# Kernel tuning notes

Hardware: AMD Instinct MI355X
Metric: run time of the kernel (lower is better)

## Reference

```python
import jax, jax.numpy as jnp
import numpy as np

N, F, H, E = 10000, 256, 256, 320000
TEMPERATURE = 1.0


def setup_inputs() -> dict:
    key = jax.random.key(0)
    k_x, k_ei, k_w1, k_b1, k_w2, k_b2 = jax.random.split(key, 6)
    x = jax.random.normal(k_x, (N, F), dtype=jnp.float32)
    edge_index = jax.random.randint(k_ei, (2, E), 0, N, dtype=jnp.int64)
    # PyTorch nn.Linear default init: U(-1/sqrt(fan_in), 1/sqrt(fan_in)), weight shape (out, in)
    lim1 = 1.0 / np.sqrt(2 * F)
    W1 = jax.random.uniform(k_w1, (H, 2 * F), dtype=jnp.float32, minval=-lim1, maxval=lim1)
    b1 = jax.random.uniform(k_b1, (H,), dtype=jnp.float32, minval=-lim1, maxval=lim1)
    lim2 = 1.0 / np.sqrt(H)
    W2 = jax.random.uniform(k_w2, (1, H), dtype=jnp.float32, minval=-lim2, maxval=lim2)
    b2 = jax.random.uniform(k_b2, (1,), dtype=jnp.float32, minval=-lim2, maxval=lim2)
    return {"x": x, "edge_index": edge_index, "W1": W1, "b1": b1, "W2": W2, "b2": b2}


def reference(x, edge_index, W1, b1, W2, b2):
    row, col = edge_index[0], edge_index[1]
    edge_feat = jnp.concatenate([x[row], x[col]], axis=-1)  # (E, 2F)
    h = jax.nn.relu(edge_feat @ W1.T + b1)                  # (E, H)
    logits = (h @ W2.T + b2).squeeze(-1)                    # (E,)
    m = jax.nn.sigmoid(logits / max(TEMPERATURE, 1e-6))
    return m
```

## Files before the change

### kernel.cpp

```cpp
#include <hip/hip_runtime.h>
#include <hip/hip_bf16.h>


typedef __attribute__((ext_vector_type(8))) short bf16x8;
typedef __attribute__((ext_vector_type(4))) float f32x4;
typedef __attribute__((ext_vector_type(2))) float f32x2;

__device__ __forceinline__ unsigned short f2bf(float f) {
    __hip_bfloat16 h = __float2bfloat16(f);
    return *reinterpret_cast<unsigned short*>(&h);
}

__device__ __forceinline__ unsigned char f2fp8(float f) {
    return (unsigned char)(__builtin_amdgcn_cvt_pk_fp8_f32(f, f, 0, false) & 0xff);
}

__global__ __launch_bounds__(256) void convert_w(const float* __restrict__ w1,
                                                 unsigned short* __restrict__ wb,
                                                 int nw4) {
    int i = blockIdx.x * 256 + threadIdx.x;
    if (i < nw4) {
        float4 v = ((const float4*)w1)[i];
        ushort4 o = {f2bf(v.x), f2bf(v.y), f2bf(v.z), f2bf(v.w)};
        ((ushort4*)wb)[i] = o;
    }
}

__global__ __launch_bounds__(256) void gemm_mfma(const float* __restrict__ x,
                                                 const unsigned short* __restrict__ wb,
                                                 const float* __restrict__ b1,
                                                 unsigned char* __restrict__ uv,
                                                 int M) {
    __shared__ __align__(16) unsigned short As[16][264];

    const int t    = threadIdx.x;
    const int wave = t >> 6;
    const int lane = t & 63;
    const int lm   = lane & 15;
    const int lq   = lane >> 4;
    const int lk   = lq * 8;
    const int m0   = blockIdx.x * 16;
    const int h    = blockIdx.y;

    {
        const int srow = t >> 4;
        const int scol = (t & 15) * 4;
        const int gr   = m0 + srow;
        const float* xr = x + (size_t)(gr < M ? gr : (M - 1)) * 256;
#pragma unroll
        for (int i = 0; i < 4; ++i) {
            float4 v = *(const float4*)(xr + scol + i * 64);
            ushort4 o = {f2bf(v.x), f2bf(v.y), f2bf(v.z), f2bf(v.w)};
            *(ushort4*)&As[srow][scol + i * 64] = o;
        }
    }
    __syncthreads();

    const unsigned short* bpre =
        wb + (size_t)(wave * 64 + lm) * 512 + h * 256 + lk;

    f32x4 acc[4];
#pragma unroll
    for (int j = 0; j < 4; ++j) acc[j] = f32x4{0.f, 0.f, 0.f, 0.f};

#pragma unroll 4
    for (int kt = 0; kt < 256; kt += 32) {
        bf16x8 a = *(const bf16x8*)&As[lm][kt + lk];
#pragma unroll
        for (int j = 0; j < 4; ++j) {
            bf16x8 b = *(const bf16x8*)(bpre + (size_t)j * 16 * 512 + kt);
            acc[j] = __builtin_amdgcn_mfma_f32_16x16x32_bf16(a, b, acc[j], 0, 0, 0);
        }
    }

    const int row0 = m0 + lq * 4;
#pragma unroll
    for (int j = 0; j < 4; ++j) {
        const int cin  = wave * 64 + j * 16 + lm;
        const int col  = h * 256 + cin;
        const float badd = h ? 0.f : b1[cin];
#pragma unroll
        for (int r = 0; r < 4; ++r) {
            if (row0 + r < M)
                uv[(size_t)(row0 + r) * 512 + col] = f2fp8(acc[j][r] + badd);
        }
    }
}

__global__ __launch_bounds__(256) void edge_kernel(const unsigned char* __restrict__ uv,
                                                   const int* __restrict__ ei,
                                                   const float* __restrict__ w2,
                                                   const float* __restrict__ b2p,
                                                   float* __restrict__ out, int E) {
    const int lane = threadIdx.x & 63;
    const int g = lane >> 4;
    const int c = lane & 15;
    const int wid  = (blockIdx.x * blockDim.x + threadIdx.x) >> 6;
    const int nwav = (gridDim.x * blockDim.x) >> 6;
    const int nb   = E >> 2;

    float w2r[16];
#pragma unroll
    for (int i = 0; i < 4; ++i)
        *(float4*)&w2r[i * 4] = *(const float4*)(w2 + c * 16 + i * 4);
    const float b2 = b2p[0];

    for (int b = wid; b < nb; b += 2 * nwav) {
        const int bB = b + nwav;
        const bool has2 = bB < nb;

        const int e0 = b * 4 + g;
        const int r0 = ei[e0];
        const int c0 = ei[E + e0];
        const int e1 = has2 ? bB * 4 + g : e0;
        const int r1 = ei[e1];
        const int c1 = ei[E + e1];

        uint4 ua = *(const uint4*)(uv + (size_t)r0 * 512 + c * 16);
        uint4 va = *(const uint4*)(uv + (size_t)c0 * 512 + 256 + c * 16);
        uint4 ub = *(const uint4*)(uv + (size_t)r1 * 512 + c * 16);
        uint4 vb = *(const uint4*)(uv + (size_t)c1 * 512 + 256 + c * 16);

        unsigned int uw[4], vw[4];
        float p;

        *(uint4*)&uw[0] = ua; *(uint4*)&vw[0] = va;
        {
            float2 p2 = {0.f, 0.f};
#pragma unroll
            for (int w = 0; w < 4; ++w) {
                f32x2 u01 = __builtin_amdgcn_cvt_pk_f32_fp8(uw[w], false);
                f32x2 u23 = __builtin_amdgcn_cvt_pk_f32_fp8(uw[w], true);
                f32x2 v01 = __builtin_amdgcn_cvt_pk_f32_fp8(vw[w], false);
                f32x2 v23 = __builtin_amdgcn_cvt_pk_f32_fp8(vw[w], true);
                float s0 = fmaxf(u01.x + v01.x, 0.f);
                float s1 = fmaxf(u01.y + v01.y, 0.f);
                float s2 = fmaxf(u23.x + v23.x, 0.f);
                float s3 = fmaxf(u23.y + v23.y, 0.f);
                p2.x = fmaf(s0, w2r[4 * w + 0], p2.x);
                p2.y = fmaf(s1, w2r[4 * w + 1], p2.y);
                p2.x = fmaf(s2, w2r[4 * w + 2], p2.x);
                p2.y = fmaf(s3, w2r[4 * w + 3], p2.y);
            }
            p = p2.x + p2.y;
        }
#pragma unroll
        for (int off = 1; off < 16; off <<= 1)
            p += __shfl_xor(p, off, 64);
        if (c == 0) out[e0] = 1.f / (1.f + __expf(-(p + b2)));

        if (has2) {
            *(uint4*)&uw[0] = ub; *(uint4*)&vw[0] = vb;
            float2 p2 = {0.f, 0.f};
#pragma unroll
            for (int w = 0; w < 4; ++w) {
                f32x2 u01 = __builtin_amdgcn_cvt_pk_f32_fp8(uw[w], false);
                f32x2 u23 = __builtin_amdgcn_cvt_pk_f32_fp8(uw[w], true);
                f32x2 v01 = __builtin_amdgcn_cvt_pk_f32_fp8(vw[w], false);
                f32x2 v23 = __builtin_amdgcn_cvt_pk_f32_fp8(vw[w], true);
                float s0 = fmaxf(u01.x + v01.x, 0.f);
                float s1 = fmaxf(u01.y + v01.y, 0.f);
                float s2 = fmaxf(u23.x + v23.x, 0.f);
                float s3 = fmaxf(u23.y + v23.y, 0.f);
                p2.x = fmaf(s0, w2r[4 * w + 0], p2.x);
                p2.y = fmaf(s1, w2r[4 * w + 1], p2.y);
                p2.x = fmaf(s2, w2r[4 * w + 2], p2.x);
                p2.y = fmaf(s3, w2r[4 * w + 3], p2.y);
            }
            p = p2.x + p2.y;
#pragma unroll
            for (int off = 1; off < 16; off <<= 1)
                p += __shfl_xor(p, off, 64);
            if (c == 0) out[e1] = 1.f / (1.f + __expf(-(p + b2)));
        }
    }
}

extern "C" void kernel_launch(void* const* d_in, const int* in_sizes, int n_in,
                              void* d_out, int out_size, void* d_ws, size_t ws_size,
                              hipStream_t stream) {
    const float* x  = (const float*)d_in[0];
    const int*   ei = (const int*)d_in[1];
    const float* W1 = (const float*)d_in[2];
    const float* b1 = (const float*)d_in[3];
    const float* W2 = (const float*)d_in[4];
    const float* b2 = (const float*)d_in[5];
    float* out = (float*)d_out;

    const int N = in_sizes[0] / 256;
    const int E = in_sizes[1] / 2;

    unsigned char*  uv = (unsigned char*)d_ws;
    unsigned short* wb = (unsigned short*)(uv + (size_t)N * 512);

    const int nw4 = (256 * 512) / 4;
    convert_w<<<(nw4 + 255) / 256, 256, 0, stream>>>(W1, wb, nw4);

    dim3 g((N + 15) / 16, 2);
    gemm_mfma<<<g, 256, 0, stream>>>(x, wb, b1, uv, N);

    edge_kernel<<<2048, 256, 0, stream>>>(uv, ei, W2, b2, out, E);
}
```

Measured before the change: 113.8 us.

## Fuse weight convert, node GEMM and edge pass into one cooperative kernel

Replaces the three separate launches (W1 bf16 conversion, per-node MFMA GEMM, per-edge gather/score) with a single persistent cooperative kernel that uses grid-wide syncs between phases. The GEMM tiles become a grid-stride loop over blocks, and the edge phase drops its two-edges-per-iteration manual unrolling. The goal is to remove launch gaps and tail effects between kernels. In exchange it adds the cost of two grid.sync barriers, fixes the grid size from an occupancy query, and loses the memory-level parallelism the two-edge unroll gave the gather phase.

```diff
diff --git a/kernel.cpp b/kernel.cpp
--- a/kernel.cpp
+++ b/kernel.cpp
@@ -1,5 +1,8 @@
 #include <hip/hip_runtime.h>
 #include <hip/hip_bf16.h>
+#include <hip/hip_cooperative_groups.h>
+
+namespace cg = cooperative_groups;
 
 
 typedef __attribute__((ext_vector_type(8))) short bf16x8;
@@ -15,88 +18,86 @@
     return (unsigned char)(__builtin_amdgcn_cvt_pk_fp8_f32(f, f, 0, false) & 0xff);
 }
 
-__global__ __launch_bounds__(256) void convert_w(const float* __restrict__ w1,
-                                                 unsigned short* __restrict__ wb,
-                                                 int nw4) {
-    int i = blockIdx.x * 256 + threadIdx.x;
-    if (i < nw4) {
-        float4 v = ((const float4*)w1)[i];
-        ushort4 o = {f2bf(v.x), f2bf(v.y), f2bf(v.z), f2bf(v.w)};
-        ((ushort4*)wb)[i] = o;
-    }
-}
-
-__global__ __launch_bounds__(256) void gemm_mfma(const float* __restrict__ x,
-                                                 const unsigned short* __restrict__ wb,
-                                                 const float* __restrict__ b1,
-                                                 unsigned char* __restrict__ uv,
-                                                 int M) {
+__global__ __launch_bounds__(256) void fused_kernel(
+        const float* __restrict__ x, const int* __restrict__ ei,
+        const float* __restrict__ W1, const float* __restrict__ b1,
+        const float* __restrict__ w2, const float* __restrict__ b2p,
+        float* __restrict__ out, unsigned char* __restrict__ uv,
+        unsigned short* __restrict__ wb, int M, int E) {
     __shared__ __align__(16) unsigned short As[16][264];
 
+    cg::grid_group grid = cg::this_grid();
     const int t    = threadIdx.x;
     const int wave = t >> 6;
     const int lane = t & 63;
     const int lm   = lane & 15;
     const int lq   = lane >> 4;
     const int lk   = lq * 8;
-    const int m0   = blockIdx.x * 16;
-    const int h    = blockIdx.y;
+    const int nblk = gridDim.x;
 
-    {
-        const int srow = t >> 4;
-        const int scol = (t & 15) * 4;
-        const int gr   = m0 + srow;
-        const float* xr = x + (size_t)(gr < M ? gr : (M - 1)) * 256;
+    for (int i = blockIdx.x * 256 + t; i < 32768; i += nblk * 256) {
+        float4 v = ((const float4*)W1)[i];
+        ushort4 o = {f2bf(v.x), f2bf(v.y), f2bf(v.z), f2bf(v.w)};
+        ((ushort4*)wb)[i] = o;
+    }
+    grid.sync();
+
+    const int ntile = ((M + 15) / 16) * 2;
+    for (int tile = blockIdx.x; tile < ntile; tile += nblk) {
+        const int h  = tile & 1;
+        const int m0 = (tile >> 1) * 16;
+
+        {
+            const int srow = t >> 4;
+            const int scol = (t & 15) * 4;
+            const int gr   = m0 + srow;
+            const float* xr = x + (size_t)(gr < M ? gr : (M - 1)) * 256;
 #pragma unroll
-        for (int i = 0; i < 4; ++i) {
-            float4 v = *(const float4*)(xr + scol + i * 64);
-            ushort4 o = {f2bf(v.x), f2bf(v.y), f2bf(v.z), f2bf(v.w)};
-            *(ushort4*)&As[srow][scol + i * 64] = o;
+            for (int i = 0; i < 4; ++i) {
+                float4 v = *(const float4*)(xr + scol + i * 64);
+                ushort4 o = {f2bf(v.x), f2bf(v.y), f2bf(v.z), f2bf(v.w)};
+                *(ushort4*)&As[srow][scol + i * 64] = o;
+            }
         }
-    }
-    __syncthreads();
+        __syncthreads();
 
-    const unsigned short* bpre =
-        wb + (size_t)(wave * 64 + lm) * 512 + h * 256 + lk;
+        const unsigned short* bpre =
+            wb + (size_t)(wave * 64 + lm) * 512 + h * 256 + lk;
 
-    f32x4 acc[4];
+        f32x4 acc[4];
 #pragma unroll
-    for (int j = 0; j < 4; ++j) acc[j] = f32x4{0.f, 0.f, 0.f, 0.f};
+        for (int j = 0; j < 4; ++j) acc[j] = f32x4{0.f, 0.f, 0.f, 0.f};
 
 #pragma unroll 4
-    for (int kt = 0; kt < 256; kt += 32) {
-        bf16x8 a = *(const bf16x8*)&As[lm][kt + lk];
+        for (int kt = 0; kt < 256; kt += 32) {
+            bf16x8 a = *(const bf16x8*)&As[lm][kt + lk];
+#pragma unroll
+            for (int j = 0; j < 4; ++j) {
+                bf16x8 b = *(const bf16x8*)(bpre + (size_t)j * 16 * 512 + kt);
+                acc[j] = __builtin_amdgcn_mfma_f32_16x16x32_bf16(a, b, acc[j], 0, 0, 0);
+            }
+        }
+
+        const int row0 = m0 + lq * 4;
 #pragma unroll
         for (int j = 0; j < 4; ++j) {
-            bf16x8 b = *(const bf16x8*)(bpre + (size_t)j * 16 * 512 + kt);
-            acc[j] = __builtin_amdgcn_mfma_f32_16x16x32_bf16(a, b, acc[j], 0, 0, 0);
+            const int cin  = wave * 64 + j * 16 + lm;
+            const int col  = h * 256 + cin;
+            const float badd = h ? 0.f : b1[cin];
+#pragma unroll
+            for (int r = 0; r < 4; ++r) {
+                if (row0 + r < M)
+                    uv[(size_t)(row0 + r) * 512 + col] = f2fp8(acc[j][r] + badd);
+            }
         }
+        __syncthreads();
     }
+    grid.sync();
 
-    const int row0 = m0 + lq * 4;
-#pragma unroll
-    for (int j = 0; j < 4; ++j) {
-        const int cin  = wave * 64 + j * 16 + lm;
-        const int col  = h * 256 + cin;
-        const float badd = h ? 0.f : b1[cin];
-#pragma unroll
-        for (int r = 0; r < 4; ++r) {
-            if (row0 + r < M)
-                uv[(size_t)(row0 + r) * 512 + col] = f2fp8(acc[j][r] + badd);
-        }
-    }
-}
-
-__global__ __launch_bounds__(256) void edge_kernel(const unsigned char* __restrict__ uv,
-                                                   const int* __restrict__ ei,
-                                                   const float* __restrict__ w2,
-                                                   const float* __restrict__ b2p,
-                                                   float* __restrict__ out, int E) {
-    const int lane = threadIdx.x & 63;
-    const int g = lane >> 4;
-    const int c = lane & 15;
-    const int wid  = (blockIdx.x * blockDim.x + threadIdx.x) >> 6;
-    const int nwav = (gridDim.x * blockDim.x) >> 6;
+    const int g = lq;
+    const int c = lm;
+    const int wid  = blockIdx.x * 4 + wave;
+    const int nwav = nblk * 4;
     const int nb   = E >> 2;
 
     float w2r[16];
@@ -105,74 +106,40 @@
         *(float4*)&w2r[i * 4] = *(const float4*)(w2 + c * 16 + i * 4);
     const float b2 = b2p[0];
 
-    for (int b = wid; b < nb; b += 2 * nwav) {
-        const int bB = b + nwav;
-        const bool has2 = bB < nb;
+    for (int b = wid; b < nb; b += nwav) {
+        const int e   = b * 4 + g;
+        const int row = ei[e];
+        const int col = ei[E + e];
 
-        const int e0 = b * 4 + g;
-        const int r0 = ei[e0];
-        const int c0 = ei[E + e0];
-        const int e1 = has2 ? bB * 4 + g : e0;
-        const int r1 = ei[e1];
-        const int c1 = ei[E + e1];
-
-        uint4 ua = *(const uint4*)(uv + (size_t)r0 * 512 + c * 16);
-        uint4 va = *(const uint4*)(uv + (size_t)c0 * 512 + 256 + c * 16);
-        uint4 ub = *(const uint4*)(uv + (size_t)r1 * 512 + c * 16);
-        uint4 vb = *(const uint4*)(uv + (size_t)c1 * 512 + 256 + c * 16);
+        uint4 ua = *(const uint4*)(uv + (size_t)row * 512 + c * 16);
+        uint4 va = *(const uint4*)(uv + (size_t)col * 512 + 256 + c * 16);
 
         unsigned int uw[4], vw[4];
-        float p;
+        *(uint4*)&uw[0] = ua; *(uint4*)&vw[0] = va;
 
-        *(uint4*)&uw[0] = ua; *(uint4*)&vw[0] = va;
-        {
-            float2 p2 = {0.f, 0.f};
+        float2 p2 = {0.f, 0.f};
 #pragma unroll
-            for (int w = 0; w < 4; ++w) {
-                f32x2 u01 = __builtin_amdgcn_cvt_pk_f32_fp8(uw[w], false);
-                f32x2 u23 = __builtin_amdgcn_cvt_pk_f32_fp8(uw[w], true);
-                f32x2 v01 = __builtin_amdgcn_cvt_pk_f32_fp8(vw[w], false);
-                f32x2 v23 = __builtin_amdgcn_cvt_pk_f32_fp8(vw[w], true);
-                float s0 = fmaxf(u01.x + v01.x, 0.f);
-                float s1 = fmaxf(u01.y + v01.y, 0.f);
-                float s2 = fmaxf(u23.x + v23.x, 0.f);
-                float s3 = fmaxf(u23.y + v23.y, 0.f);
-                p2.x = fmaf(s0, w2r[4 * w + 0], p2.x);
-                p2.y = fmaf(s1, w2r[4 * w + 1], p2.y);
-                p2.x = fmaf(s2, w2r[4 * w + 2], p2.x);
-                p2.y = fmaf(s3, w2r[4 * w + 3], p2.y);
-            }
-            p = p2.x + p2.y;
+        for (int w = 0; w < 4; ++w) {
+            f32x2 u01 = __builtin_amdgcn_cvt_pk_f32_fp8(uw[w], false);
+            f32x2 u23 = __builtin_amdgcn_cvt_pk_f32_fp8(uw[w], true);
+            f32x2 v01 = __builtin_amdgcn_cvt_pk_f32_fp8(vw[w], false);
+            f32x2 v23 = __builtin_amdgcn_cvt_pk_f32_fp8(vw[w], true);
+            float s0 = fmaxf(u01.x + v01.x, 0.f);
+            float s1 = fmaxf(u01.y + v01.y, 0.f);
+            float s2 = fmaxf(u23.x + v23.x, 0.f);
+            float s3 = fmaxf(u23.y + v23.y, 0.f);
+            p2.x = fmaf(s0, w2r[4 * w + 0], p2.x);
+            p2.y = fmaf(s1, w2r[4 * w + 1], p2.y);
+            p2.x = fmaf(s2, w2r[4 * w + 2], p2.x);
+            p2.y = fmaf(s3, w2r[4 * w + 3], p2.y);
         }
+        float p = p2.x + p2.y;
+
 #pragma unroll
         for (int off = 1; off < 16; off <<= 1)
             p += __shfl_xor(p, off, 64);
-        if (c == 0) out[e0] = 1.f / (1.f + __expf(-(p + b2)));
 
-        if (has2) {
-            *(uint4*)&uw[0] = ub; *(uint4*)&vw[0] = vb;
-            float2 p2 = {0.f, 0.f};
-#pragma unroll
-            for (int w = 0; w < 4; ++w) {
-                f32x2 u01 = __builtin_amdgcn_cvt_pk_f32_fp8(uw[w], false);
-                f32x2 u23 = __builtin_amdgcn_cvt_pk_f32_fp8(uw[w], true);
-                f32x2 v01 = __builtin_amdgcn_cvt_pk_f32_fp8(vw[w], false);
-                f32x2 v23 = __builtin_amdgcn_cvt_pk_f32_fp8(vw[w], true);
-                float s0 = fmaxf(u01.x + v01.x, 0.f);
-                float s1 = fmaxf(u01.y + v01.y, 0.f);
-                float s2 = fmaxf(u23.x + v23.x, 0.f);
-                float s3 = fmaxf(u23.y + v23.y, 0.f);
-                p2.x = fmaf(s0, w2r[4 * w + 0], p2.x);
-                p2.y = fmaf(s1, w2r[4 * w + 1], p2.y);
-                p2.x = fmaf(s2, w2r[4 * w + 2], p2.x);
-                p2.y = fmaf(s3, w2r[4 * w + 3], p2.y);
-            }
-            p = p2.x + p2.y;
-#pragma unroll
-            for (int off = 1; off < 16; off <<= 1)
-                p += __shfl_xor(p, off, 64);
-            if (c == 0) out[e1] = 1.f / (1.f + __expf(-(p + b2)));
-        }
+        if (c == 0) out[e] = 1.f / (1.f + __expf(-(p + b2)));
     }
 }
 
@@ -187,17 +154,23 @@
     const float* b2 = (const float*)d_in[5];
     float* out = (float*)d_out;
 
-    const int N = in_sizes[0] / 256;
-    const int E = in_sizes[1] / 2;
+    int N = in_sizes[0] / 256;
+    int E = in_sizes[1] / 2;
 
     unsigned char*  uv = (unsigned char*)d_ws;
     unsigned short* wb = (unsigned short*)(uv + (size_t)N * 512);
 
-    const int nw4 = (256 * 512) / 4;
-    convert_w<<<(nw4 + 255) / 256, 256, 0, stream>>>(W1, wb, nw4);
+    int maxBlk = 0;
+    hipOccupancyMaxActiveBlocksPerMultiprocessor(&maxBlk,
+                                                 (const void*)fused_kernel,
+                                                 256, 0);
+    if (maxBlk < 1) maxBlk = 1;
+    if (maxBlk > 8) maxBlk = 8;
+    int grid = maxBlk * 256;
 
-    dim3 g((N + 15) / 16, 2);
-    gemm_mfma<<<g, 256, 0, stream>>>(x, wb, b1, uv, N);
-
-    edge_kernel<<<2048, 256, 0, stream>>>(uv, ei, W2, b2, out, E);
+    void* args[] = {(void*)&x, (void*)&ei, (void*)&W1, (void*)&b1, (void*)&W2,
+                    (void*)&b2, (void*)&out, (void*)&uv, (void*)&wb,
+                    (void*)&N, (void*)&E};
+    hipLaunchCooperativeKernel((void*)fused_kernel, dim3(grid), dim3(256),
+                               args, 0, stream);
 }
```

Measured after the change: 250.0 us. 120% more time.
